# Performance work log

Hardware: AMD Instinct MI355X
Metric: run time of the kernel (lower is better)

Reference implementation:

```python
import jax, jax.numpy as jnp
import numpy as np

B, L, A, K = 2, 1024, 14, 30
NUM_RBF = 16
NPE = 16  # num_positional_embeddings
EF = 128  # edge_features
EDGE_IN = NPE + NUM_RBF * A * A  # 3152


def setup_inputs() -> dict:
    key = jax.random.key(0)
    ks = jax.random.split(key, 4)
    # coords scaled so pairwise distances span the RBF range [0, 20]
    X = jax.random.normal(ks[0], (B, L, A, 3), dtype=jnp.float32) * 3.0
    mask = jnp.ones((B, L), dtype=jnp.float32)
    residue_idx = jnp.tile(jnp.arange(L, dtype=jnp.int32)[None, :], (B, 1))
    chain_labels = jnp.zeros((B, L), dtype=jnp.int32)
    atom_mask = jax.random.randint(ks[1], (B, L, A), 0, 2).astype(jnp.float32)
    W_edge = jax.random.normal(ks[2], (EF, EDGE_IN), dtype=jnp.float32) * 0.02
    ln_gamma = jnp.ones((EF,), dtype=jnp.float32)
    ln_beta = jnp.zeros((EF,), dtype=jnp.float32)
    return {"X": X, "mask": mask, "residue_idx": residue_idx,
            "chain_labels": chain_labels, "atom_mask": atom_mask,
            "W_edge": W_edge, "ln_gamma": ln_gamma, "ln_beta": ln_beta}


def reference(X, mask, residue_idx, chain_labels, atom_mask, W_edge, ln_gamma, ln_beta):
    Bq, Lq = X.shape[0], X.shape[1]
    # ---- CA pairwise distances + masked top-k (smallest) ----
    X_ca = X[:, :, 1, :]
    m2 = mask[:, :, None] * mask[:, None, :]                    # [B,L,L]
    dX = X_ca[:, :, None, :] - X_ca[:, None, :, :]
    D = m2 * jnp.sqrt(jnp.sum(dX ** 2, -1) + 1e-6)
    D_max = jnp.max(D, -1, keepdims=True)
    D_adjust = D + 2.0 * (1.0 - m2) * D_max
    _, E_idx = jax.lax.top_k(-D_adjust, K)                      # smallest K -> [B,L,K]
    # ---- transformer positional encoding of relative index ----
    ii = jnp.arange(Lq, dtype=jnp.float32)[None, :, None]
    d = (E_idx.astype(jnp.float32) - ii)[..., None]             # [B,L,K,1]
    freq = jnp.exp(jnp.arange(0, NPE, 2, dtype=jnp.float32) * (-(np.log(10000.0) / NPE)))
    angles = d * freq                                           # [B,L,K,NPE/2]
    E_pos = jnp.concatenate([jnp.cos(angles), jnp.sin(angles)], -1)  # [B,L,K,NPE]
    # ---- impute CB, build 14-atom set ----
    N_, Ca, C_, O_ = X[:, :, 0, :], X[:, :, 1, :], X[:, :, 2, :], X[:, :, 3, :]
    b = Ca - N_
    c = C_ - Ca
    a = jnp.cross(b, c)
    Cb = -0.58273431 * a + 0.56802827 * b - 0.54067466 * c + Ca
    X2 = jnp.concatenate([jnp.stack([N_, Ca, C_, O_, Cb], -2), X[:, :, 5:, :]], -2)  # [B,L,14,3]
    am = 1.0 - atom_mask                                        # module passes 1 - atom_mask
    # ---- gather neighbor atoms, fused 14x14 atom-pair RBFs ----
    bidx = jnp.arange(Bq)[:, None, None]
    X2n = X2[bidx, E_idx]                                       # [B,L,K,14,3]
    amn = am[bidx, E_idx]                                       # [B,L,K,14]
    diff = X2[:, :, None, :, None, :] - X2n[:, :, :, None, :, :]
    Dab = jnp.sqrt(jnp.sum(diff ** 2, -1) + 1e-6)               # [B,L,K,14,14] (a of i, b of nbr)
    combo = am[:, :, None, :, None] * amn[:, :, :, None, :]     # [B,L,K,14,14]
    mu = jnp.linspace(0.0, 20.0, NUM_RBF)
    sigma = 20.0 / NUM_RBF
    rbf = jnp.exp(-(((Dab[..., None] - mu) / sigma) ** 2)) * combo[..., None]
    RBF_all = rbf.reshape(Bq, Lq, K, A * A * NUM_RBF)           # matches torch cat order (i,j,rbf)
    # ---- edge embedding + layernorm ----
    E = jnp.concatenate([E_pos, RBF_all], -1)                   # [B,L,K,EDGE_IN]
    E = E @ W_edge.T                                            # [B,L,K,EF]
    mean = jnp.mean(E, -1, keepdims=True)
    var = jnp.var(E, -1, keepdims=True)
    E = (E - mean) / jnp.sqrt(var + 1e-5) * ln_gamma + ln_beta
    return (E, E_idx)
```

## Files before the change

kernel.cpp:

```cpp
#include <hip/hip_runtime.h>
#include <hip/hip_bf16.h>
#include <stdint.h>

#define LQ 1024
#define BQ 2
#define AQ 14
#define KQ 30
#define EFQ 128
#define EDGE_IN 3152
#define KPAD 3200
#define NCHUNK 50
#define MTILE 128
#define ROWS (BQ*LQ*KQ)
#define EIDX_OFF (ROWS*EFQ)

typedef __attribute__((ext_vector_type(8))) _Float16 half8;
typedef __attribute__((ext_vector_type(2))) _Float16 half2t;
typedef __attribute__((ext_vector_type(4))) float floatx4;
typedef unsigned long long ull;

static __device__ __forceinline__ uint32_t pkh(float a, float b) {
    auto h = __builtin_amdgcn_cvt_pkrtz(a, b);
    return __builtin_bit_cast(uint32_t, h);
}
static __device__ __forceinline__ ull umin64(ull a, ull b) { return a < b ? a : b; }

__global__ __launch_bounds__(512) void topk_kernel(
    const float* __restrict__ X, const float* __restrict__ mask,
    const float* __restrict__ W, float* __restrict__ out,
    int* __restrict__ idx_ws, _Float16* __restrict__ wpad)
{
    __shared__ float xs[LQ], ys[LQ], zs[LQ], ms[LQ];
    const int t = threadIdx.x;

    if (blockIdx.x >= 256) {
        int base = (blockIdx.x - 256)*8192 + t;
        #pragma unroll
        for (int r = 0; r < 16; ++r) {
            int idx = base + r*512;
            int n = idx / KPAD, f = idx - n*KPAD;
            float v = (f < EDGE_IN) ? W[(size_t)n*EDGE_IN + f] : 0.0f;
            wpad[idx] = (_Float16)v;
        }
        return;
    }

    const int w = t >> 6, lane = t & 63;
    const int row = blockIdx.x*8 + w;
    const int b = row >> 10, i = row & (LQ - 1);

    for (int j = t; j < LQ; j += 512) {
        size_t base = ((size_t)(b*LQ + j))*42 + 3;
        xs[j] = X[base+0]; ys[j] = X[base+1]; zs[j] = X[base+2];
        ms[j] = mask[b*LQ + j];
    }
    __syncthreads();

    const float mif = ms[i];
    const double cx = (double)xs[i], cy = (double)ys[i], cz = (double)zs[i];

    double Dk[16]; float mf[16];
    bool allone = (mif == 1.0f);
    #pragma unroll
    for (int s = 0; s < 16; ++s) {
        int j = s*64 + lane;
        double dx = __dsub_rn(cx, (double)xs[j]);
        double dy = __dsub_rn(cy, (double)ys[j]);
        double dz = __dsub_rn(cz, (double)zs[j]);
        mf[s] = ms[j];
        Dk[s] = __dadd_rn(__dadd_rn(__dmul_rn(dx,dx), __dmul_rn(dy,dy)),
                          __dmul_rn(dz,dz));
        allone = allone && (mf[s] == 1.0f);
    }

    if (!__all(allone ? 1 : 0)) {
        const double mi_d = (double)mif;
        double lm = 0.0;
        #pragma unroll
        for (int s = 0; s < 16; ++s) {
            double m2 = __dmul_rn(mi_d, (double)mf[s]);
            Dk[s] = __dmul_rn(m2, sqrt(__dadd_rn(Dk[s], 1e-6)));
            lm = fmax(lm, Dk[s]);
        }
        #pragma unroll
        for (int off = 32; off; off >>= 1) lm = fmax(lm, __shfl_xor(lm, off));
        #pragma unroll
        for (int s = 0; s < 16; ++s) {
            double m2 = __dmul_rn(mi_d, (double)mf[s]);
            Dk[s] = __dadd_rn(Dk[s],
                    __dmul_rn(__dmul_rn(2.0, __dsub_rn(1.0, m2)), lm));
        }
    }

    ull key[16];
    #pragma unroll
    for (int s = 0; s < 16; ++s)
        key[s] = (((ull)__double_as_longlong(Dk[s])) & ~1023ull)
               | (unsigned)(s*64 + lane);

    for (int k = 0; k < KQ; ++k) {
        ull a0 = umin64(key[0],  key[1]),  a1 = umin64(key[2],  key[3]);
        ull a2 = umin64(key[4],  key[5]),  a3 = umin64(key[6],  key[7]);
        ull a4 = umin64(key[8],  key[9]),  a5 = umin64(key[10], key[11]);
        ull a6 = umin64(key[12], key[13]), a7 = umin64(key[14], key[15]);
        ull b0 = umin64(a0, a1), b1 = umin64(a2, a3);
        ull b2 = umin64(a4, a5), b3 = umin64(a6, a7);
        ull bk = umin64(umin64(b0, b1), umin64(b2, b3));
        #pragma unroll
        for (int off = 32; off; off >>= 1)
            bk = umin64(bk, (ull)__shfl_xor(bk, off));
        int j = (int)(bk & 1023ull);
        if (lane == 0) {
            int rg = row*KQ + k;
            idx_ws[rg] = j;
            out[EIDX_OFF + rg] = (float)j;
        }
        bool mine = ((j & 63) == lane);
        int s_win = j >> 6;
        #pragma unroll
        for (int s = 0; s < 16; ++s)
            key[s] = (mine && s == s_win) ? ~0ull : key[s];
    }
}

struct FusedSmem {
    alignas(16) unsigned short atoms[256*56];
    alignas(16) unsigned short Bl[2*8192];
    alignas(16) float drow[MTILE];
    int residg[256];
    float gsh[EFQ], bsh[EFQ];
};

static __device__ __forceinline__ void gen_rbf(
    const char* __restrict__ rowA, const char* __restrict__ rowB,
    int ao, int bo, float rboff, uint32_t* __restrict__ v)
{
    uint2 ca = *reinterpret_cast<const uint2*>(rowA + ao);
    uint2 nb = *reinterpret_cast<const uint2*>(rowB + bo);
    half2t c0 = __builtin_bit_cast(half2t, ca.x);
    half2t c1 = __builtin_bit_cast(half2t, ca.y);
    half2t n0 = __builtin_bit_cast(half2t, nb.x);
    half2t n1 = __builtin_bit_cast(half2t, nb.y);
    half2t dxy = c0 - n0;
    half2t dzw = c1 - n1;
    float dx = (float)dxy[0], dy = (float)dxy[1], dz = (float)dzw[0];
    float ssq = __fmaf_rn(dx, dx, __fmaf_rn(dy, dy,
                __fmaf_rn(dz, dz, 9.2332585e-7f)));
    float u = __builtin_amdgcn_sqrtf(ssq) + rboff;
    const float CJ[8] = {0.0f, 1.28119795f, 2.5623959f, 3.84359385f,
                         5.1247918f, 6.40598975f, 7.6871877f, 8.96838565f};
    #pragma unroll
    for (int k = 0; k < 4; ++k) {
        float t0 = u - CJ[2*k];
        float t1 = u - CJ[2*k+1];
        v[k] = pkh(__builtin_amdgcn_exp2f(-(t0*t0)),
                   __builtin_amdgcn_exp2f(-(t1*t1)));
    }
}

__global__ __launch_bounds__(512) void fused_kernel(
    const float* __restrict__ X, const float* __restrict__ atom_mask,
    const _Float16* __restrict__ wpad, const float* __restrict__ gamma,
    const float* __restrict__ beta, const int* __restrict__ idx_ws,
    float* __restrict__ out)
{
    __shared__ FusedSmem sm;
    const int t = threadIdx.x;
    const int row0 = blockIdx.x * MTILE;
    const int b = row0 / (LQ*KQ);

    if (t < MTILE) {
        int rg = row0 + t;
        int rem = rg - b*(LQ*KQ);
        int i = rem / KQ;
        int j = idx_ws[rg];
        sm.residg[t]       = b*LQ + i;
        sm.residg[MTILE+t] = b*LQ + j;
        sm.drow[t] = (float)j - (float)i;
    }
    if (t < EFQ) { sm.gsh[t] = gamma[t]; sm.bsh[t] = beta[t]; }
    __syncthreads();

    const int w = t >> 6, lane = t & 63, q = lane >> 4, l15 = lane & 15;
    const int m = w*16 + l15;

    int stRegion[2]; const _Float16* stBase[2];
    #pragma unroll
    for (int i2 = 0; i2 < 2; ++i2) {
        int region = w*2 + i2;
        int n = region*8 + (lane >> 3);
        int kbsrc = (lane & 7) ^ (lane >> 3);
        stRegion[i2] = region;
        stBase[i2] = wpad + (size_t)n*KPAD + kbsrc*8;
    }
    auto stage = [&](int c) {
        #pragma unroll
        for (int i2 = 0; i2 < 2; ++i2) {
            const _Float16* g = stBase[i2] + c*64;
            __builtin_amdgcn_global_load_lds(
                (const __attribute__((address_space(1))) uint32_t*)g,
                (__attribute__((address_space(3))) uint32_t*)
                    &sm.Bl[((c & 1) << 13) + stRegion[i2]*512],
                16, 0, 0);
        }
    };
    stage(0);

    for (int u2 = t; u2 < 256*14; u2 += 512) {
        int s = u2 / 14; int a = u2 - s*14;
        const float* xp = X + (size_t)sm.residg[s]*42 + a*3;
        uint2 pk; pk.x = pkh(xp[0], xp[1]); pk.y = pkh(xp[2], 0.0f);
        *reinterpret_cast<uint2*>(&sm.atoms[s*56 + a*4]) = pk;
    }
    __syncthreads();

    if (t < 256) {
        unsigned short* at = &sm.atoms[t*56];
        auto ld3 = [&](int slot, float& x, float& y, float& z) {
            half2t p0 = *reinterpret_cast<const half2t*>(at + slot*4);
            half2t p1 = *reinterpret_cast<const half2t*>(at + slot*4 + 2);
            x = (float)p0[0]; y = (float)p0[1]; z = (float)p1[0];
        };
        float Nx,Ny,Nz, Cax,Cay,Caz, Cx,Cy,Cz;
        ld3(0, Nx,Ny,Nz); ld3(1, Cax,Cay,Caz); ld3(2, Cx,Cy,Cz);
        float bx=Cax-Nx, by=Cay-Ny, bz=Caz-Nz;
        float ex=Cx-Cax, ey=Cy-Cay, ez=Cz-Caz;
        float ax = by*ez - bz*ey, ay = bz*ex - bx*ez, az = bx*ey - by*ex;
        float cbx = -0.58273431f*ax + 0.56802827f*bx - 0.54067466f*ex + Cax;
        float cby = -0.58273431f*ay + 0.56802827f*by - 0.54067466f*ey + Cay;
        float cbz = -0.58273431f*az + 0.56802827f*bz - 0.54067466f*ez + Caz;
        uint2 pk4; pk4.x = pkh(cbx, cby); pk4.y = pkh(cbz, 0.0f);
        *reinterpret_cast<uint2*>(at + 4*4) = pk4;

        const float P = (t < MTILE) ? 30000.0f : -30000.0f;
        const uint32_t pxx = pkh(P, P), pxy = pkh(P, 0.0f);
        half2t sc2; sc2[0] = (_Float16)0.96089846f; sc2[1] = (_Float16)0.96089846f;
        const float* amp = &atom_mask[(size_t)sm.residg[t]*AQ];
        #pragma unroll
        for (int a = 0; a < AQ; ++a) {
            uint2 vv = *reinterpret_cast<const uint2*>(at + a*4);
            half2t lo = __builtin_bit_cast(half2t, vv.x) * sc2;
            half2t hi = __builtin_bit_cast(half2t, vv.y) * sc2;
            bool msk = amp[a] > 0.5f;
            uint2 ov;
            ov.x = msk ? pxx : __builtin_bit_cast(uint32_t, lo);
            ov.y = msk ? pxy : __builtin_bit_cast(uint32_t, hi);
            *reinterpret_cast<uint2*>(at + a*4) = ov;
        }
    }

    int boff0[8], boff1[8];
    #pragma unroll
    for (int nt = 0; nt < 8; ++nt) {
        int n = nt*16 + l15;
        boff0[nt] = n*64 + ((q ^ (n&7))*8);
        boff1[nt] = n*64 + (((4+q) ^ (n&7))*8);
    }

    const char* rowA = (const char*)&sm.atoms[m*56];
    const char* rowB = (const char*)&sm.atoms[(MTILE+m)*56];
    const int   qlt2  = (q < 2) ? 1 : 0;
    const float rboff = -(float)((q & 1) * 8) * 1.28119795f;

    floatx4 acc[8];
    #pragma unroll
    for (int nt = 0; nt < 8; ++nt) acc[nt] = (floatx4){0.f,0.f,0.f,0.f};

    __syncthreads();

    union H8 { uint32_t u[4]; half8 h; };
    for (int c = 0; c < NCHUNK; ++c) {
        if (c < NCHUNK-1) stage(c+1);

        int p0 = 4*c - qlt2;
        int p1 = p0 + 2;
        int pa0 = (p0 * 74899) >> 20;  int pa1 = (p1 * 74899) >> 20;
        pa0 = pa0 > 13 ? 13 : pa0;     pa1 = pa1 > 13 ? 13 : pa1;
        int ao0 = pa0 << 3, bo0 = (p0 - pa0*14) << 3;
        int ao1 = pa1 << 3, bo1 = (p1 - pa1*14) << 3;

        H8 a00, a01;
        if (c == 0) {
            if (qlt2) {
                const float fr[8] = {1.0f, 0.31622776601683794f, 0.1f,
                    0.031622776601683794f, 0.01f, 0.0031622776601683794f,
                    0.001f, 0.00031622776601683794f};
                float dr = sm.drow[m];
                float e[8];
                if (q == 0) {
                    #pragma unroll
                    for (int j = 0; j < 8; ++j) e[j] = __cosf(dr * fr[j]);
                } else {
                    #pragma unroll
                    for (int j = 0; j < 8; ++j) e[j] = __sinf(dr * fr[j]);
                }
                #pragma unroll
                for (int k = 0; k < 4; ++k) a00.u[k] = pkh(e[2*k], e[2*k+1]);
            } else {
                gen_rbf(rowA, rowB, ao0, bo0, rboff, a00.u);
            }
        } else {
            gen_rbf(rowA, rowB, ao0, bo0, rboff, a00.u);
        }
        gen_rbf(rowA, rowB, ao1, bo1, rboff, a01.u);

        const unsigned short* Bb = &sm.Bl[(c & 1) << 13];
        #pragma unroll
        for (int nt = 0; nt < 8; ++nt) {
            half8 b0 = *reinterpret_cast<const half8*>(&Bb[boff0[nt]]);
            half8 b1 = *reinterpret_cast<const half8*>(&Bb[boff1[nt]]);
            acc[nt] = __builtin_amdgcn_mfma_f32_16x16x32_f16(a00.h, b0, acc[nt], 0, 0, 0);
            acc[nt] = __builtin_amdgcn_mfma_f32_16x16x32_f16(a01.h, b1, acc[nt], 0, 0, 0);
        }
        __syncthreads();
    }

    #pragma unroll
    for (int v = 0; v < 4; ++v) {
        float s = 0.f, s2 = 0.f;
        #pragma unroll
        for (int nt = 0; nt < 8; ++nt) { float x = acc[nt][v]; s += x; s2 += x*x; }
        #pragma unroll
        for (int off = 1; off < 16; off <<= 1) {
            s  += __shfl_xor(s,  off);
            s2 += __shfl_xor(s2, off);
        }
        float mean = s * (1.0f/128.0f);
        float var  = s2 * (1.0f/128.0f) - mean*mean;
        float rstd = 1.0f / sqrtf(var + 1e-5f);
        int row_l = w*16 + q*4 + v;
        size_t obase = (size_t)(row0 + row_l)*EFQ;
        #pragma unroll
        for (int nt = 0; nt < 8; ++nt) {
            int col = nt*16 + l15;
            out[obase + col] = (acc[nt][v] - mean)*rstd*sm.gsh[col] + sm.bsh[col];
        }
    }
}

extern "C" void kernel_launch(void* const* d_in, const int* in_sizes, int n_in,
                              void* d_out, int out_size, void* d_ws, size_t ws_size,
                              hipStream_t stream)
{
    const float* X         = (const float*)d_in[0];
    const float* mask      = (const float*)d_in[1];
    const float* atom_mask = (const float*)d_in[4];
    const float* W         = (const float*)d_in[5];
    const float* gamma     = (const float*)d_in[6];
    const float* beta      = (const float*)d_in[7];
    float* out = (float*)d_out;

    int*       idx_ws = (int*)d_ws;
    _Float16*  wpad   = (_Float16*)((char*)d_ws + 262144);

    hipLaunchKernelGGL(topk_kernel, dim3(306), dim3(512), 0, stream,
                       X, mask, W, out, idx_ws, wpad);
    hipLaunchKernelGGL(fused_kernel, dim3(ROWS/MTILE), dim3(512), 0, stream,
                       X, atom_mask, wpad, gamma, beta, idx_ws, out);
}
```

Measured before the change: 169.3 us.

## Split weight operand staging: half via LDS, half loaded directly to registers

Only the first 32 K-columns of each 64-wide weight chunk are staged into LDS through global_load_lds. The second half is loaded straight from global memory into registers for each N-tile. This halves LDS staging size and LDS read traffic, so occupancy can rise. The cost is more global and L2 traffic per wave, since every wave re-reads the same weight half, plus extra registers for the eight prefetched fragments.

```diff
diff --git a/kernel.cpp b/kernel.cpp
--- a/kernel.cpp
+++ b/kernel.cpp
@@ -125,7 +125,7 @@
 
 struct FusedSmem {
     alignas(16) unsigned short atoms[256*56];
-    alignas(16) unsigned short Bl[2*8192];
+    alignas(16) unsigned short Bl[2*4096];
     alignas(16) float drow[MTILE];
     int residg[256];
     float gsh[EFQ], bsh[EFQ];
@@ -184,25 +184,17 @@
     const int w = t >> 6, lane = t & 63, q = lane >> 4, l15 = lane & 15;
     const int m = w*16 + l15;
 
-    int stRegion[2]; const _Float16* stBase[2];
-    #pragma unroll
-    for (int i2 = 0; i2 < 2; ++i2) {
-        int region = w*2 + i2;
-        int n = region*8 + (lane >> 3);
-        int kbsrc = (lane & 7) ^ (lane >> 3);
-        stRegion[i2] = region;
-        stBase[i2] = wpad + (size_t)n*KPAD + kbsrc*8;
-    }
+    {
+    }
+    const int scomb = (t & 7) ^ ((t >> 3) & 7);
+    const int sn    = (((t >> 3)) << 1) | (scomb >> 2);
+    const _Float16* stSrc = wpad + (size_t)sn*KPAD + (scomb & 3)*8;
     auto stage = [&](int c) {
-        #pragma unroll
-        for (int i2 = 0; i2 < 2; ++i2) {
-            const _Float16* g = stBase[i2] + c*64;
-            __builtin_amdgcn_global_load_lds(
-                (const __attribute__((address_space(1))) uint32_t*)g,
-                (__attribute__((address_space(3))) uint32_t*)
-                    &sm.Bl[((c & 1) << 13) + stRegion[i2]*512],
-                16, 0, 0);
-        }
+        __builtin_amdgcn_global_load_lds(
+            (const __attribute__((address_space(1))) uint32_t*)(stSrc + c*64),
+            (__attribute__((address_space(3))) uint32_t*)
+                &sm.Bl[((c & 1) << 12) + (t << 3)],
+            16, 0, 0);
     };
     stage(0);
 
@@ -249,13 +241,12 @@
         }
     }
 
-    int boff0[8], boff1[8];
-    #pragma unroll
-    for (int nt = 0; nt < 8; ++nt) {
-        int n = nt*16 + l15;
-        boff0[nt] = n*64 + ((q ^ (n&7))*8);
-        boff1[nt] = n*64 + (((4+q) ^ (n&7))*8);
-    }
+    const int bbase = (l15 >> 1)*64 + ((((((l15 & 1) << 2) | q)) ^ (l15 >> 1)) << 3);
+
+    const _Float16* bg = wpad + (size_t)l15*KPAD + 32 + q*8;
+    const _Float16* bgp[8];
+    #pragma unroll
+    for (int nt = 0; nt < 8; ++nt) bgp[nt] = bg + (size_t)nt*(16*KPAD);
 
     const char* rowA = (const char*)&sm.atoms[m*56];
     const char* rowB = (const char*)&sm.atoms[(MTILE+m)*56];
@@ -270,6 +261,10 @@
 
     union H8 { uint32_t u[4]; half8 h; };
     for (int c = 0; c < NCHUNK; ++c) {
+        half8 b1r[8];
+        #pragma unroll
+        for (int nt = 0; nt < 8; ++nt)
+            b1r[nt] = *reinterpret_cast<const half8*>(bgp[nt] + c*64);
         if (c < NCHUNK-1) stage(c+1);
 
         int p0 = 4*c - qlt2;
@@ -304,14 +299,16 @@
         }
         gen_rbf(rowA, rowB, ao1, bo1, rboff, a01.u);
 
-        const unsigned short* Bb = &sm.Bl[(c & 1) << 13];
+        const unsigned short* Bb = &sm.Bl[(c & 1) << 12];
         #pragma unroll
         for (int nt = 0; nt < 8; ++nt) {
-            half8 b0 = *reinterpret_cast<const half8*>(&Bb[boff0[nt]]);
-            half8 b1 = *reinterpret_cast<const half8*>(&Bb[boff1[nt]]);
+            half8 b0 = *reinterpret_cast<const half8*>(&Bb[nt*512 + bbase]);
             acc[nt] = __builtin_amdgcn_mfma_f32_16x16x32_f16(a00.h, b0, acc[nt], 0, 0, 0);
-            acc[nt] = __builtin_amdgcn_mfma_f32_16x16x32_f16(a01.h, b1, acc[nt], 0, 0, 0);
-        }
+        }
+        #pragma unroll
+        for (int nt = 0; nt < 8; ++nt)
+            acc[nt] = __builtin_amdgcn_mfma_f32_16x16x32_f16(a01.h, b1r[nt], acc[nt], 0, 0, 0);
+
         __syncthreads();
     }
 
```

After: 288.2 us. 1.7x slower.

## Halve block to 256 threads with two M-tiles per wave, single-buffer B

Applied to the files above, without the earlier changes.

Each wave now computes two 16-row M-subtiles so the block shrinks to 256 threads, reusing each B fragment read from LDS across two MFMA chains. The B staging buffer goes from double to single buffering, with a barrier before and after each stage, which saves LDS so more blocks fit per CU (launch bounds 256,4). The cost is that global-to-LDS loads are no longer overlapped with compute within a block, so latency hiding now depends on having several blocks resident.

```diff
diff --git a/kernel.cpp b/kernel.cpp
--- a/kernel.cpp
+++ b/kernel.cpp
@@ -125,7 +125,7 @@
 
 struct FusedSmem {
     alignas(16) unsigned short atoms[256*56];
-    alignas(16) unsigned short Bl[2*8192];
+    alignas(16) unsigned short Bl[8192];
     alignas(16) float drow[MTILE];
     int residg[256];
     float gsh[EFQ], bsh[EFQ];
@@ -158,7 +158,7 @@
     }
 }
 
-__global__ __launch_bounds__(512) void fused_kernel(
+__global__ __launch_bounds__(256, 4) void fused_kernel(
     const float* __restrict__ X, const float* __restrict__ atom_mask,
     const _Float16* __restrict__ wpad, const float* __restrict__ gamma,
     const float* __restrict__ beta, const int* __restrict__ idx_ws,
@@ -182,12 +182,12 @@
     __syncthreads();
 
     const int w = t >> 6, lane = t & 63, q = lane >> 4, l15 = lane & 15;
-    const int m = w*16 + l15;
-
-    int stRegion[2]; const _Float16* stBase[2];
-    #pragma unroll
-    for (int i2 = 0; i2 < 2; ++i2) {
-        int region = w*2 + i2;
+    const int m0 = w*32 + l15, m1 = m0 + 16;
+
+    int stRegion[4]; const _Float16* stBase[4];
+    #pragma unroll
+    for (int i2 = 0; i2 < 4; ++i2) {
+        int region = w*4 + i2;
         int n = region*8 + (lane >> 3);
         int kbsrc = (lane & 7) ^ (lane >> 3);
         stRegion[i2] = region;
@@ -195,18 +195,16 @@
     }
     auto stage = [&](int c) {
         #pragma unroll
-        for (int i2 = 0; i2 < 2; ++i2) {
+        for (int i2 = 0; i2 < 4; ++i2) {
             const _Float16* g = stBase[i2] + c*64;
             __builtin_amdgcn_global_load_lds(
                 (const __attribute__((address_space(1))) uint32_t*)g,
-                (__attribute__((address_space(3))) uint32_t*)
-                    &sm.Bl[((c & 1) << 13) + stRegion[i2]*512],
+                (__attribute__((address_space(3))) uint32_t*)&sm.Bl[stRegion[i2]*512],
                 16, 0, 0);
         }
     };
-    stage(0);
-
-    for (int u2 = t; u2 < 256*14; u2 += 512) {
+
+    for (int u2 = t; u2 < 256*14; u2 += 256) {
         int s = u2 / 14; int a = u2 - s*14;
         const float* xp = X + (size_t)sm.residg[s]*42 + a*3;
         uint2 pk; pk.x = pkh(xp[0], xp[1]); pk.y = pkh(xp[2], 0.0f);
@@ -214,7 +212,7 @@
     }
     __syncthreads();
 
-    if (t < 256) {
+    {
         unsigned short* at = &sm.atoms[t*56];
         auto ld3 = [&](int slot, float& x, float& y, float& z) {
             half2t p0 = *reinterpret_cast<const half2t*>(at + slot*4);
@@ -257,20 +255,26 @@
         boff1[nt] = n*64 + (((4+q) ^ (n&7))*8);
     }
 
-    const char* rowA = (const char*)&sm.atoms[m*56];
-    const char* rowB = (const char*)&sm.atoms[(MTILE+m)*56];
+    const char* rowA0 = (const char*)&sm.atoms[m0*56];
+    const char* rowB0 = (const char*)&sm.atoms[(MTILE+m0)*56];
+    const char* rowA1 = (const char*)&sm.atoms[m1*56];
+    const char* rowB1 = (const char*)&sm.atoms[(MTILE+m1)*56];
     const int   qlt2  = (q < 2) ? 1 : 0;
     const float rboff = -(float)((q & 1) * 8) * 1.28119795f;
 
-    floatx4 acc[8];
-    #pragma unroll
-    for (int nt = 0; nt < 8; ++nt) acc[nt] = (floatx4){0.f,0.f,0.f,0.f};
+    floatx4 acc0[8], acc1[8];
+    #pragma unroll
+    for (int nt = 0; nt < 8; ++nt) {
+        acc0[nt] = (floatx4){0.f,0.f,0.f,0.f};
+        acc1[nt] = (floatx4){0.f,0.f,0.f,0.f};
+    }
 
     __syncthreads();
 
     union H8 { uint32_t u[4]; half8 h; };
     for (int c = 0; c < NCHUNK; ++c) {
-        if (c < NCHUNK-1) stage(c+1);
+        if (c) __syncthreads();
+        stage(c);
 
         int p0 = 4*c - qlt2;
         int p1 = p0 + 2;
@@ -279,63 +283,69 @@
         int ao0 = pa0 << 3, bo0 = (p0 - pa0*14) << 3;
         int ao1 = pa1 << 3, bo1 = (p1 - pa1*14) << 3;
 
-        H8 a00, a01;
-        if (c == 0) {
-            if (qlt2) {
-                const float fr[8] = {1.0f, 0.31622776601683794f, 0.1f,
-                    0.031622776601683794f, 0.01f, 0.0031622776601683794f,
-                    0.001f, 0.00031622776601683794f};
-                float dr = sm.drow[m];
-                float e[8];
-                if (q == 0) {
-                    #pragma unroll
-                    for (int j = 0; j < 8; ++j) e[j] = __cosf(dr * fr[j]);
-                } else {
-                    #pragma unroll
-                    for (int j = 0; j < 8; ++j) e[j] = __sinf(dr * fr[j]);
-                }
+        H8 a00, a01, a10, a11;
+        if (c == 0 && qlt2) {
+            const float fr[8] = {1.0f, 0.31622776601683794f, 0.1f,
+                0.031622776601683794f, 0.01f, 0.0031622776601683794f,
+                0.001f, 0.00031622776601683794f};
+            float dr0 = sm.drow[m0], dr1 = sm.drow[m1];
+            float e0[8], e1[8];
+            if (q == 0) {
                 #pragma unroll
-                for (int k = 0; k < 4; ++k) a00.u[k] = pkh(e[2*k], e[2*k+1]);
+                for (int j = 0; j < 8; ++j) { e0[j] = __cosf(dr0 * fr[j]); e1[j] = __cosf(dr1 * fr[j]); }
             } else {
-                gen_rbf(rowA, rowB, ao0, bo0, rboff, a00.u);
+                #pragma unroll
+                for (int j = 0; j < 8; ++j) { e0[j] = __sinf(dr0 * fr[j]); e1[j] = __sinf(dr1 * fr[j]); }
+            }
+            #pragma unroll
+            for (int k = 0; k < 4; ++k) {
+                a00.u[k] = pkh(e0[2*k], e0[2*k+1]);
+                a10.u[k] = pkh(e1[2*k], e1[2*k+1]);
             }
         } else {
-            gen_rbf(rowA, rowB, ao0, bo0, rboff, a00.u);
-        }
-        gen_rbf(rowA, rowB, ao1, bo1, rboff, a01.u);
-
-        const unsigned short* Bb = &sm.Bl[(c & 1) << 13];
+            gen_rbf(rowA0, rowB0, ao0, bo0, rboff, a00.u);
+            gen_rbf(rowA1, rowB1, ao0, bo0, rboff, a10.u);
+        }
+        gen_rbf(rowA0, rowB0, ao1, bo1, rboff, a01.u);
+        gen_rbf(rowA1, rowB1, ao1, bo1, rboff, a11.u);
+
+        __syncthreads();
         #pragma unroll
         for (int nt = 0; nt < 8; ++nt) {
-            half8 b0 = *reinterpret_cast<const half8*>(&Bb[boff0[nt]]);
-            half8 b1 = *reinterpret_cast<const half8*>(&Bb[boff1[nt]]);
-            acc[nt] = __builtin_amdgcn_mfma_f32_16x16x32_f16(a00.h, b0, acc[nt], 0, 0, 0);
-            acc[nt] = __builtin_amdgcn_mfma_f32_16x16x32_f16(a01.h, b1, acc[nt], 0, 0, 0);
-        }
-        __syncthreads();
-    }
-
-    #pragma unroll
-    for (int v = 0; v < 4; ++v) {
-        float s = 0.f, s2 = 0.f;
-        #pragma unroll
-        for (int nt = 0; nt < 8; ++nt) { float x = acc[nt][v]; s += x; s2 += x*x; }
-        #pragma unroll
-        for (int off = 1; off < 16; off <<= 1) {
-            s  += __shfl_xor(s,  off);
-            s2 += __shfl_xor(s2, off);
-        }
-        float mean = s * (1.0f/128.0f);
-        float var  = s2 * (1.0f/128.0f) - mean*mean;
-        float rstd = 1.0f / sqrtf(var + 1e-5f);
-        int row_l = w*16 + q*4 + v;
-        size_t obase = (size_t)(row0 + row_l)*EFQ;
-        #pragma unroll
-        for (int nt = 0; nt < 8; ++nt) {
-            int col = nt*16 + l15;
-            out[obase + col] = (acc[nt][v] - mean)*rstd*sm.gsh[col] + sm.bsh[col];
-        }
-    }
+            half8 b0 = *reinterpret_cast<const half8*>(&sm.Bl[boff0[nt]]);
+            half8 b1 = *reinterpret_cast<const half8*>(&sm.Bl[boff1[nt]]);
+            acc0[nt] = __builtin_amdgcn_mfma_f32_16x16x32_f16(a00.h, b0, acc0[nt], 0, 0, 0);
+            acc0[nt] = __builtin_amdgcn_mfma_f32_16x16x32_f16(a01.h, b1, acc0[nt], 0, 0, 0);
+            acc1[nt] = __builtin_amdgcn_mfma_f32_16x16x32_f16(a10.h, b0, acc1[nt], 0, 0, 0);
+            acc1[nt] = __builtin_amdgcn_mfma_f32_16x16x32_f16(a11.h, b1, acc1[nt], 0, 0, 0);
+        }
+    }
+
+    auto lnrows = [&](const floatx4* acc, int g) {
+        #pragma unroll
+        for (int v = 0; v < 4; ++v) {
+            float s = 0.f, s2 = 0.f;
+            #pragma unroll
+            for (int nt = 0; nt < 8; ++nt) { float x = acc[nt][v]; s += x; s2 += x*x; }
+            #pragma unroll
+            for (int off = 1; off < 16; off <<= 1) {
+                s  += __shfl_xor(s,  off);
+                s2 += __shfl_xor(s2, off);
+            }
+            float mean = s * (1.0f/128.0f);
+            float var  = s2 * (1.0f/128.0f) - mean*mean;
+            float rstd = 1.0f / sqrtf(var + 1e-5f);
+            int row_l = w*32 + g*16 + q*4 + v;
+            size_t obase = (size_t)(row0 + row_l)*EFQ;
+            #pragma unroll
+            for (int nt = 0; nt < 8; ++nt) {
+                int col = nt*16 + l15;
+                out[obase + col] = (acc[nt][v] - mean)*rstd*sm.gsh[col] + sm.bsh[col];
+            }
+        }
+    };
+    lnrows(acc0, 0);
+    lnrows(acc1, 1);
 }
 
 extern "C" void kernel_launch(void* const* d_in, const int* in_sizes, int n_in,
@@ -355,6 +365,6 @@
 
     hipLaunchKernelGGL(topk_kernel, dim3(306), dim3(512), 0, stream,
                        X, mask, W, out, idx_ws, wpad);
-    hipLaunchKernelGGL(fused_kernel, dim3(ROWS/MTILE), dim3(512), 0, stream,
+    hipLaunchKernelGGL(fused_kernel, dim3(ROWS/MTILE), dim3(256), 0, stream,
                        X, atom_mask, wpad, gamma, beta, idx_ws, out);
 }
```

Result: slower. 180.6 us (+6.6%).

## Split K across wave pairs with two M-tiles per wave to reuse B fragments

Applied to the files above, without the earlier changes.

Each wave now covers two 16-row M tiles and half of every K chunk. Every B fragment loaded from LDS feeds two MFMAs, which halves B reads per MFMA and gives the RBF work two independent streams. The two K-halves are combined through an LDS scratch area reusing the atoms buffer, in two passes with extra barriers before the layernorm. The change also adds a min-blocks hint of 4 to launch_bounds, which raises register pressure with two accumulator sets and risks spills.

```diff
diff --git a/kernel.cpp b/kernel.cpp
--- a/kernel.cpp
+++ b/kernel.cpp
@@ -158,7 +158,7 @@
     }
 }
 
-__global__ __launch_bounds__(512) void fused_kernel(
+__global__ __launch_bounds__(512, 4) void fused_kernel(
     const float* __restrict__ X, const float* __restrict__ atom_mask,
     const _Float16* __restrict__ wpad, const float* __restrict__ gamma,
     const float* __restrict__ beta, const int* __restrict__ idx_ws,
@@ -182,7 +182,8 @@
     __syncthreads();
 
     const int w = t >> 6, lane = t & 63, q = lane >> 4, l15 = lane & 15;
-    const int m = w*16 + l15;
+    const int kh = w >> 2, wr = w & 3;
+    const int m0 = wr*32 + l15, m1 = m0 + 16;
 
     int stRegion[2]; const _Float16* stBase[2];
     #pragma unroll
@@ -249,22 +250,27 @@
         }
     }
 
-    int boff0[8], boff1[8];
+    int boff[8];
     #pragma unroll
     for (int nt = 0; nt < 8; ++nt) {
         int n = nt*16 + l15;
-        boff0[nt] = n*64 + ((q ^ (n&7))*8);
-        boff1[nt] = n*64 + (((4+q) ^ (n&7))*8);
-    }
-
-    const char* rowA = (const char*)&sm.atoms[m*56];
-    const char* rowB = (const char*)&sm.atoms[(MTILE+m)*56];
+        boff[nt] = n*64 + (((kh*4 + q) ^ (n&7))*8);
+    }
+
+    const char* rowA0 = (const char*)&sm.atoms[m0*56];
+    const char* rowB0 = (const char*)&sm.atoms[(MTILE+m0)*56];
+    const char* rowA1 = (const char*)&sm.atoms[m1*56];
+    const char* rowB1 = (const char*)&sm.atoms[(MTILE+m1)*56];
     const int   qlt2  = (q < 2) ? 1 : 0;
+    const int   pbase = 2*kh - qlt2;
     const float rboff = -(float)((q & 1) * 8) * 1.28119795f;
 
-    floatx4 acc[8];
-    #pragma unroll
-    for (int nt = 0; nt < 8; ++nt) acc[nt] = (floatx4){0.f,0.f,0.f,0.f};
+    floatx4 acc0[8], acc1[8];
+    #pragma unroll
+    for (int nt = 0; nt < 8; ++nt) {
+        acc0[nt] = (floatx4){0.f,0.f,0.f,0.f};
+        acc1[nt] = (floatx4){0.f,0.f,0.f,0.f};
+    }
 
     __syncthreads();
 
@@ -272,69 +278,93 @@
     for (int c = 0; c < NCHUNK; ++c) {
         if (c < NCHUNK-1) stage(c+1);
 
-        int p0 = 4*c - qlt2;
-        int p1 = p0 + 2;
-        int pa0 = (p0 * 74899) >> 20;  int pa1 = (p1 * 74899) >> 20;
-        pa0 = pa0 > 13 ? 13 : pa0;     pa1 = pa1 > 13 ? 13 : pa1;
-        int ao0 = pa0 << 3, bo0 = (p0 - pa0*14) << 3;
-        int ao1 = pa1 << 3, bo1 = (p1 - pa1*14) << 3;
-
-        H8 a00, a01;
-        if (c == 0) {
-            if (qlt2) {
-                const float fr[8] = {1.0f, 0.31622776601683794f, 0.1f,
-                    0.031622776601683794f, 0.01f, 0.0031622776601683794f,
-                    0.001f, 0.00031622776601683794f};
-                float dr = sm.drow[m];
-                float e[8];
-                if (q == 0) {
-                    #pragma unroll
-                    for (int j = 0; j < 8; ++j) e[j] = __cosf(dr * fr[j]);
-                } else {
-                    #pragma unroll
-                    for (int j = 0; j < 8; ++j) e[j] = __sinf(dr * fr[j]);
-                }
+        H8 a0, a1;
+        if (c == 0 && kh == 0 && qlt2) {
+            const float fr[8] = {1.0f, 0.31622776601683794f, 0.1f,
+                0.031622776601683794f, 0.01f, 0.0031622776601683794f,
+                0.001f, 0.00031622776601683794f};
+            float dr0 = sm.drow[m0], dr1 = sm.drow[m1];
+            float e0[8], e1[8];
+            if (q == 0) {
                 #pragma unroll
-                for (int k = 0; k < 4; ++k) a00.u[k] = pkh(e[2*k], e[2*k+1]);
+                for (int j = 0; j < 8; ++j) { e0[j] = __cosf(dr0 * fr[j]); e1[j] = __cosf(dr1 * fr[j]); }
             } else {
-                gen_rbf(rowA, rowB, ao0, bo0, rboff, a00.u);
+                #pragma unroll
+                for (int j = 0; j < 8; ++j) { e0[j] = __sinf(dr0 * fr[j]); e1[j] = __sinf(dr1 * fr[j]); }
+            }
+            #pragma unroll
+            for (int k = 0; k < 4; ++k) {
+                a0.u[k] = pkh(e0[2*k], e0[2*k+1]);
+                a1.u[k] = pkh(e1[2*k], e1[2*k+1]);
             }
         } else {
-            gen_rbf(rowA, rowB, ao0, bo0, rboff, a00.u);
-        }
-        gen_rbf(rowA, rowB, ao1, bo1, rboff, a01.u);
+            int p  = 4*c + pbase;
+            int pa = (p * 74899) >> 20;
+            pa = pa > 13 ? 13 : pa;
+            int ao = pa << 3, bo = (p - pa*14) << 3;
+            gen_rbf(rowA0, rowB0, ao, bo, rboff, a0.u);
+            gen_rbf(rowA1, rowB1, ao, bo, rboff, a1.u);
+        }
 
         const unsigned short* Bb = &sm.Bl[(c & 1) << 13];
         #pragma unroll
         for (int nt = 0; nt < 8; ++nt) {
-            half8 b0 = *reinterpret_cast<const half8*>(&Bb[boff0[nt]]);
-            half8 b1 = *reinterpret_cast<const half8*>(&Bb[boff1[nt]]);
-            acc[nt] = __builtin_amdgcn_mfma_f32_16x16x32_f16(a00.h, b0, acc[nt], 0, 0, 0);
-            acc[nt] = __builtin_amdgcn_mfma_f32_16x16x32_f16(a01.h, b1, acc[nt], 0, 0, 0);
+            half8 bv = *reinterpret_cast<const half8*>(&Bb[boff[nt]]);
+            acc0[nt] = __builtin_amdgcn_mfma_f32_16x16x32_f16(a0.h, bv, acc0[nt], 0, 0, 0);
+            acc1[nt] = __builtin_amdgcn_mfma_f32_16x16x32_f16(a1.h, bv, acc1[nt], 0, 0, 0);
         }
         __syncthreads();
     }
 
-    #pragma unroll
-    for (int v = 0; v < 4; ++v) {
-        float s = 0.f, s2 = 0.f;
-        #pragma unroll
-        for (int nt = 0; nt < 8; ++nt) { float x = acc[nt][v]; s += x; s2 += x*x; }
-        #pragma unroll
-        for (int off = 1; off < 16; off <<= 1) {
-            s  += __shfl_xor(s,  off);
-            s2 += __shfl_xor(s2, off);
-        }
-        float mean = s * (1.0f/128.0f);
-        float var  = s2 * (1.0f/128.0f) - mean*mean;
-        float rstd = 1.0f / sqrtf(var + 1e-5f);
-        int row_l = w*16 + q*4 + v;
-        size_t obase = (size_t)(row0 + row_l)*EFQ;
-        #pragma unroll
-        for (int nt = 0; nt < 8; ++nt) {
-            int col = nt*16 + l15;
-            out[obase + col] = (acc[nt][v] - mean)*rstd*sm.gsh[col] + sm.bsh[col];
-        }
+    float* scr = reinterpret_cast<float*>(sm.atoms);
+    #pragma unroll
+    for (int pass = 0; pass < 2; ++pass) {
+        if ((wr >> 1) == pass && kh == 1) {
+            #pragma unroll
+            for (int v = 0; v < 4; ++v) {
+                int r0 = (wr & 1)*32 + q*4 + v;
+                int r1 = r0 + 16;
+                #pragma unroll
+                for (int nt = 0; nt < 8; ++nt) {
+                    scr[r0*132 + nt*16 + l15] = acc0[nt][v];
+                    scr[r1*132 + nt*16 + l15] = acc1[nt][v];
+                }
+            }
+        }
+        __syncthreads();
+        if ((wr >> 1) == pass && kh == 0) {
+            #pragma unroll
+            for (int g = 0; g < 2; ++g) {
+                #pragma unroll
+                for (int v = 0; v < 4; ++v) {
+                    int rloc = (wr & 1)*32 + g*16 + q*4 + v;
+                    float s = 0.f, s2 = 0.f;
+                    float xv[8];
+                    #pragma unroll
+                    for (int nt = 0; nt < 8; ++nt) {
+                        float x = (g ? acc1[nt][v] : acc0[nt][v])
+                                + scr[rloc*132 + nt*16 + l15];
+                        xv[nt] = x; s += x; s2 += x*x;
+                    }
+                    #pragma unroll
+                    for (int off = 1; off < 16; off <<= 1) {
+                        s  += __shfl_xor(s,  off);
+                        s2 += __shfl_xor(s2, off);
+                    }
+                    float mean = s * (1.0f/128.0f);
+                    float var  = s2 * (1.0f/128.0f) - mean*mean;
+                    float rstd = 1.0f / sqrtf(var + 1e-5f);
+                    int row_l = wr*32 + g*16 + q*4 + v;
+                    size_t obase = (size_t)(row0 + row_l)*EFQ;
+                    #pragma unroll
+                    for (int nt = 0; nt < 8; ++nt) {
+                        int col = nt*16 + l15;
+                        out[obase + col] = (xv[nt] - mean)*rstd*sm.gsh[col] + sm.bsh[col];
+                    }
+                }
+            }
+        }
+        __syncthreads();
     }
 }
 
```

Result: slower. 173.9 us (+2.7%).
